# Performance work log

Measured on AMD Instinct MI355X. Metric: run time of the kernel, lower is better.

Reference implementation:

```python
import jax, jax.numpy as jnp
import numpy as np
from math import sqrt

B, S, D, H = 4, 2048, 1024, 16
DH = D // H          # 64
DF = 4 * D           # 4096
EPS = 1e-5
NEG = -1e9


def layer_norm(x, w, b):
    mu = jnp.mean(x, axis=-1, keepdims=True)
    var = jnp.mean((x - mu) ** 2, axis=-1, keepdims=True)
    return (x - mu) * jax.lax.rsqrt(var + EPS) * w + b


def setup_inputs() -> dict:
    key = jax.random.key(0)
    ks = jax.random.split(key, 16)
    s = 0.02
    return {
        "state": jax.random.normal(ks[0], (B, S, D), jnp.float32),
        "mask": jax.random.randint(ks[1], (B, S), 0, 2, jnp.int32),
        "ln1_w": jnp.ones((D,), jnp.float32),
        "ln1_b": jnp.zeros((D,), jnp.float32),
        "Wq": jax.random.normal(ks[2], (H, D, DH), jnp.float32) * s,
        "bq": jnp.zeros((H, DH), jnp.float32),
        "Wk": jax.random.normal(ks[3], (H, D, DH), jnp.float32) * s,
        "bk": jnp.zeros((H, DH), jnp.float32),
        "Wv": jax.random.normal(ks[4], (H, D, DH), jnp.float32) * s,
        "bv": jnp.zeros((H, DH), jnp.float32),
        "Wo": jax.random.normal(ks[5], (D, D), jnp.float32) * s,
        "bo": jnp.zeros((D,), jnp.float32),
        "ln2_w": jnp.ones((D,), jnp.float32),
        "ln2_b": jnp.zeros((D,), jnp.float32),
        "W1": jax.random.normal(ks[6], (D, DF), jnp.float32) * s,
        "b1": jnp.zeros((DF,), jnp.float32),
        "W2": jax.random.normal(ks[7], (DF, D), jnp.float32) * s,
        "b2": jnp.zeros((D,), jnp.float32),
    }


def reference(state, mask, ln1_w, ln1_b, Wq, bq, Wk, bk, Wv, bv, Wo, bo,
              ln2_w, ln2_b, W1, b1, W2, b2):
    # pre-norm attention block
    hidden = layer_norm(state, ln1_w, ln1_b)               # [B,S,D]
    q = jnp.einsum("bsd,hde->bhse", hidden, Wq) + bq[None, :, None, :]
    k = jnp.einsum("bsd,hde->bhse", hidden, Wk) + bk[None, :, None, :]
    v = jnp.einsum("bsd,hde->bhse", hidden, Wv) + bv[None, :, None, :]
    scores = jnp.einsum("bhse,bhte->bhst", q, k) / sqrt(DH)  # [B,H,S,S]
    scores = jnp.where(mask[:, None, None, :] == 0, NEG, scores)
    weights = jax.nn.softmax(scores, axis=-1)
    attended = jnp.einsum("bhst,bhte->bhse", weights, v)    # [B,H,S,DH]
    # concat heads in head order (matches torch cat over per-head outputs)
    attended = attended.transpose(0, 2, 1, 3).reshape(B, S, D)
    attn_out = attended @ Wo + bo
    output = state + attn_out
    # pre-norm FFN block (dropout=0 -> identity)
    hidden = layer_norm(output, ln2_w, ln2_b)
    ff = jax.nn.gelu(hidden @ W1 + b1, approximate=False) @ W2 + b2
    return output + ff
```

## Files before the change

### kernel.cpp

```cpp
#include <hip/hip_runtime.h>
#include <math.h>

#define B_  4
#define S_  2048
#define D_  1024
#define H_  16
#define DH_ 64
#define DF_ 4096
#define M_  8192

#define QSC 0.18033688011112042f

typedef __attribute__((ext_vector_type(8))) short bf8_t;
typedef __attribute__((ext_vector_type(4))) float f4_t;

#if defined(__has_builtin)
#if __has_builtin(__builtin_amdgcn_cvt_pk_bf16_f32)
#define HAVE_PKCVT 1
#endif
#if __has_builtin(__builtin_amdgcn_global_load_lds)
#define HAVE_ASYNC 1
#endif
#if __has_builtin(__builtin_amdgcn_exp2f)
#define EXP2F(x) __builtin_amdgcn_exp2f(x)
#else
#define EXP2F(x) __expf((x) * 0.69314718055994531f)
#endif
#else
#define EXP2F(x) __expf((x) * 0.69314718055994531f)
#endif

__device__ __forceinline__ unsigned pk_bf16(float lo, float hi) {
#ifdef HAVE_PKCVT
  auto r = __builtin_amdgcn_cvt_pk_bf16_f32(lo, hi);
  unsigned u; __builtin_memcpy(&u, &r, 4); return u;
#else
  union { float f; unsigned u; } a, b2; a.f = lo; b2.f = hi;
  unsigned ra = a.u + 0x7fffu + ((a.u >> 16) & 1u);
  unsigned rb = b2.u + 0x7fffu + ((b2.u >> 16) & 1u);
  return (ra >> 16) | (rb & 0xffff0000u);
#endif
}

__device__ __forceinline__ unsigned short f2bf(float x) {
  return (unsigned short)(pk_bf16(x, x) & 0xffffu);
}

__device__ __forceinline__ bf8_t upk8(unsigned u0, unsigned u1, unsigned u2, unsigned u3) {
  union { unsigned u[4]; bf8_t v; } c;
  c.u[0] = u0; c.u[1] = u1; c.u[2] = u2; c.u[3] = u3; return c.v;
}

__device__ __forceinline__ f4_t mfma32(bf8_t a, bf8_t b, f4_t c) {
  return __builtin_amdgcn_mfma_f32_16x16x32_bf16(a, b, c, 0, 0, 0);
}

__device__ __forceinline__ void async16(const void* g, void* l) {
#ifdef HAVE_ASYNC
  __builtin_amdgcn_global_load_lds((__attribute__((address_space(1))) void*)(g),
                                   (__attribute__((address_space(3))) void*)(l), 16, 0, 0);
#else
  *(uint4*)l = *(const uint4*)g;
#endif
}

__device__ __forceinline__ int sw(int row) { return row & 7; }


__global__ __launch_bounds__(256) void wtrans_kernel(const float* __restrict__ in,
                                                     unsigned short* __restrict__ out,
                                                     int K, int N) {
  const int k0 = blockIdx.x * 32, n0 = blockIdx.y * 32;
  __shared__ float t[32][33];
  const int tid = threadIdx.x;
#pragma unroll
  for (int i = 0; i < 4; i++) {
    int idx = i * 256 + tid; int r = idx >> 5, c = idx & 31;
    t[r][c] = in[(size_t)(k0 + r) * N + n0 + c];
  }
  __syncthreads();
#pragma unroll
  for (int i = 0; i < 4; i++) {
    int idx = i * 256 + tid; int r = idx >> 5, c = idx & 31;
    out[(size_t)(n0 + r) * K + k0 + c] = f2bf(t[c][r]);
  }
}

__global__ __launch_bounds__(256) void qkvpack_kernel(const float* __restrict__ Wq,
                                                      const float* __restrict__ Wk,
                                                      const float* __restrict__ Wv,
                                                      unsigned short* __restrict__ WqkvT) {
  const int z = blockIdx.z;
  const int sel = z >> 4, h = z & 15;
  const float* in = (sel == 0 ? Wq : sel == 1 ? Wk : Wv) + (size_t)h * D_ * DH_;
  const int k0 = blockIdx.x * 32, n0 = blockIdx.y * 32;
  __shared__ float t[32][33];
  const int tid = threadIdx.x;
#pragma unroll
  for (int i = 0; i < 4; i++) {
    int idx = i * 256 + tid; int r = idx >> 5, c = idx & 31;
    t[r][c] = in[(size_t)(k0 + r) * DH_ + n0 + c];
  }
  __syncthreads();
#pragma unroll
  for (int i = 0; i < 4; i++) {
    int idx = i * 256 + tid; int r = idx >> 5, c = idx & 31;
    int n = sel * 1024 + h * 64 + n0 + r;
    WqkvT[(size_t)n * D_ + k0 + c] = f2bf(t[c][r]);
  }
}

__global__ void biaspack_kernel(const float* __restrict__ bq, const float* __restrict__ bk,
                                const float* __restrict__ bv, float* __restrict__ bqkv) {
  int i = blockIdx.x * 256 + threadIdx.x;
  if (i < 3072) {
    int sel = i >> 10, j = i & 1023;
    const float* src = sel == 0 ? bq : sel == 1 ? bk : bv;
    bqkv[i] = src[j];
  }
}


__global__ __launch_bounds__(256) void ln_kernel(const float* __restrict__ x,
                                                 const float* __restrict__ w,
                                                 const float* __restrict__ bb,
                                                 unsigned short* __restrict__ out) {
  const int row = blockIdx.x;
  const float* xr = x + (size_t)row * D_;
  const int tid = threadIdx.x;
  float v[4]; float s = 0.f;
#pragma unroll
  for (int i = 0; i < 4; i++) { v[i] = xr[tid + i * 256]; s += v[i]; }
  __shared__ float red[8];
#pragma unroll
  for (int o = 32; o; o >>= 1) s += __shfl_xor(s, o, 64);
  const int wv = tid >> 6, ln = tid & 63;
  if (!ln) red[wv] = s;
  __syncthreads();
  float mean = (red[0] + red[1] + red[2] + red[3]) * (1.f / 1024.f);
  float s2 = 0.f;
#pragma unroll
  for (int i = 0; i < 4; i++) { float d = v[i] - mean; s2 += d * d; }
#pragma unroll
  for (int o = 32; o; o >>= 1) s2 += __shfl_xor(s2, o, 64);
  if (!ln) red[4 + wv] = s2;
  __syncthreads();
  float var = (red[4] + red[5] + red[6] + red[7]) * (1.f / 1024.f);
  float rstd = rsqrtf(var + 1e-5f);
#pragma unroll
  for (int i = 0; i < 4; i++) {
    int c = tid + i * 256;
    out[(size_t)row * D_ + c] = f2bf((v[i] - mean) * rstd * w[c] + bb[c]);
  }
}

__global__ __launch_bounds__(256) void ffn2red_kernel(float* __restrict__ out,
                                                      const float* __restrict__ P,
                                                      const float* __restrict__ resid,
                                                      const float* __restrict__ bias) {
  const size_t i = ((size_t)blockIdx.x * 256 + threadIdx.x) * 4;
  f4_t a  = *(const f4_t*)&out[i];
  f4_t p  = *(const f4_t*)&P[i];
  f4_t rr = *(const f4_t*)&resid[i];
  f4_t bb = *(const f4_t*)&bias[(int)(i & 1023)];
  *(f4_t*)&out[i] = a + p + rr + bb;
}

template <int EPI>
__global__ __launch_bounds__(256) void gemm_bt(const unsigned short* __restrict__ A,
                                               const unsigned short* __restrict__ Bt,
                                               const float* __restrict__ bias,
                                               const float* __restrict__ resid,
                                               unsigned short* __restrict__ outb,
                                               float* __restrict__ outf,
                                               int Ndim, int Kdim) {
  __shared__ __align__(16) unsigned short Asmem[4096];
  __shared__ __align__(16) unsigned short Bsmem[4096];
  const int tid = threadIdx.x;
  const int wave = tid >> 6, lane = tid & 63;
  const int quad = lane >> 4, l16 = lane & 15;
  const int wm = wave >> 1, wn = wave & 1;

  const int gx = gridDim.x;
  const int nwg = gx * (int)gridDim.y;
  const int lin = (int)blockIdx.y * gx + (int)blockIdx.x;
  const int swz = (lin & 7) * (nwg >> 3) + (lin >> 3);
  const int m0 = (swz / gx) * 128, n0 = (swz % gx) * 128;

  const f4_t fzero = {0.f, 0.f, 0.f, 0.f};
  f4_t acc[4][4];
#pragma unroll
  for (int i = 0; i < 4; i++)
#pragma unroll
    for (int j = 0; j < 4; j++) acc[i][j] = fzero;

  const int rowA = tid >> 2;
  const int kp = (tid & 3) * 8;

  for (int k0 = 0; k0 < Kdim; k0 += 32) {
    __syncthreads();
#pragma unroll
    for (int r = 0; r < 2; r++) {
      const int row = r * 64 + rowA;
      const int e = row * 32 + kp;
      async16(A  + (size_t)(m0 + row) * Kdim + k0 + kp, &Asmem[e]);
      async16(Bt + (size_t)(n0 + row) * Kdim + k0 + kp, &Bsmem[e]);
    }
    __syncthreads();

    bf8_t a[4], b[4];
#pragma unroll
    for (int i = 0; i < 4; i++) {
      a[i] = *(const bf8_t*)&Asmem[(wm * 64 + i * 16 + l16) * 32 + quad * 8];
      b[i] = *(const bf8_t*)&Bsmem[(wn * 64 + i * 16 + l16) * 32 + quad * 8];
    }
#pragma unroll
    for (int i = 0; i < 4; i++)
#pragma unroll
      for (int j = 0; j < 4; j++)
        acc[i][j] = mfma32(a[i], b[j], acc[i][j]);
  }

#pragma unroll
  for (int i = 0; i < 4; i++) {
#pragma unroll
    for (int j = 0; j < 4; j++) {
#pragma unroll
      for (int r = 0; r < 4; r++) {
        const int m = m0 + wm * 64 + i * 16 + quad * 4 + r;
        const int n = n0 + wn * 64 + j * 16 + l16;
        float v = acc[i][j][r] + bias[n];
        if constexpr (EPI == 2) v = 0.5f * v * (1.f + erff(v * 0.70710678118654752f));
        if constexpr (EPI == 1) {
          v += resid[(size_t)m * Ndim + n];
          outf[(size_t)m * Ndim + n] = v;
        } else {
          outb[(size_t)m * Ndim + n] = f2bf(v);
        }
      }
    }
  }
}

template <int EPI>
__global__ __launch_bounds__(512, 2) void gemm256(const unsigned short* __restrict__ A,
                                                  const unsigned short* __restrict__ Bt,
                                                  const float* __restrict__ bias,
                                                  const float* __restrict__ resid,
                                                  unsigned short* __restrict__ outb,
                                                  float* __restrict__ outf,
                                                  float* __restrict__ outf2,
                                                  unsigned short* __restrict__ vTout,
                                                  int Ndim, int Kdim, int Kstride) {
  __shared__ __align__(16) unsigned short Asm[32768];
  __shared__ __align__(16) unsigned short Bsm[32768];
  const int tid = threadIdx.x;
  const int wave = tid >> 6, lane = tid & 63;
  const int quad = lane >> 4, l16 = lane & 15;
  const int wm = wave >> 2, wn = wave & 3;

  const int gx = gridDim.x;
  const int nwg = gx * (int)gridDim.y;
  const int lin = (int)blockIdx.y * gx + (int)blockIdx.x;
  const int swz = (lin & 7) * (nwg >> 3) + (lin >> 3);
  const int m0 = (swz / gx) * 256, n0 = (swz % gx) * 256;
  const int kz = (int)blockIdx.z * Kdim;

  const int NT = Kdim >> 6;
  const int srow = lane >> 3, schk = lane & 7;

#define STAGE_A(t, row0) do {                                               \
    const int r_ = (row0) + srow;                                           \
    async16(A + (size_t)(m0 + r_) * Kstride + kz + (t) * 64 +               \
                ((schk ^ (r_ & 7)) << 3),                                   \
            &Asm[(((t) & 1) << 14) + ((row0) << 6)]); } while (0)
#define STAGE_B(t, row0) do {                                               \
    const int r_ = (row0) + srow;                                           \
    async16(Bt + (size_t)(n0 + r_) * Kstride + kz + (t) * 64 +              \
                 ((schk ^ (r_ & 7)) << 3),                                  \
            &Bsm[(((t) & 1) << 14) + ((row0) << 6)]); } while (0)
#define STAGE_FULL(t) do {                                                  \
    STAGE_A(t, wave * 8);       STAGE_A(t, 64 + wave * 8);                  \
    STAGE_A(t, 128 + wave * 8); STAGE_A(t, 192 + wave * 8);                 \
    STAGE_B(t, wave * 8);       STAGE_B(t, 64 + wave * 8);                  \
    STAGE_B(t, 128 + wave * 8); STAGE_B(t, 192 + wave * 8); } while (0)

#define AFR(bo, row, s) \
  (*(const bf8_t*)&Asm[(bo) + ((row) << 6) + ((((s) * 4 + quad) ^ ((row) & 7)) << 3)])
#define BFR(bo, row, s) \
  (*(const bf8_t*)&Bsm[(bo) + ((row) << 6) + ((((s) * 4 + quad) ^ ((row) & 7)) << 3)])

  const f4_t fzero = {0.f, 0.f, 0.f, 0.f};
  f4_t acc[8][4];
#pragma unroll
  for (int i = 0; i < 8; i++)
#pragma unroll
    for (int j = 0; j < 4; j++) acc[i][j] = fzero;

  STAGE_FULL(0);
  STAGE_FULL(1);
  asm volatile("s_waitcnt vmcnt(8)" ::: "memory");
  __builtin_amdgcn_s_barrier();

  const int ar0 = wm << 7;
  const int br0 = wn << 6;

  for (int t = 0; t < NT; ++t) {
    const int bo = (t & 1) << 14;
    const bool pf = (t + 2) < NT;
    const int t2 = t + 2;
    bf8_t a0[8], b0[4], a1[8], b1[4];

#pragma unroll
    for (int i = 0; i < 8; i++) a0[i] = AFR(bo, ar0 + i * 16 + l16, 0);
#pragma unroll
    for (int j = 0; j < 4; j++) b0[j] = BFR(bo, br0 + j * 16 + l16, 0);
#pragma unroll
    for (int i = 0; i < 8; i++) a1[i] = AFR(bo, ar0 + i * 16 + l16, 1);
#pragma unroll
    for (int j = 0; j < 4; j++) b1[j] = BFR(bo, br0 + j * 16 + l16, 1);

    __builtin_amdgcn_s_setprio(1);
#pragma unroll
    for (int i = 0; i < 8; i++)
#pragma unroll
      for (int j = 0; j < 4; j++)
        acc[i][j] = mfma32(a0[i], b0[j], acc[i][j]);
    __builtin_amdgcn_s_setprio(0);

    asm volatile("s_waitcnt lgkmcnt(0)" ::: "memory");
    __builtin_amdgcn_s_barrier();

    if (pf) STAGE_FULL(t2);

    __builtin_amdgcn_s_setprio(1);
#pragma unroll
    for (int i = 0; i < 8; i++)
#pragma unroll
      for (int j = 0; j < 4; j++)
        acc[i][j] = mfma32(a1[i], b1[j], acc[i][j]);
    __builtin_amdgcn_s_setprio(0);

    if (pf) asm volatile("s_waitcnt vmcnt(8)" ::: "memory");
    else    asm volatile("s_waitcnt vmcnt(0)" ::: "memory");
    __builtin_amdgcn_s_barrier();
  }

#undef STAGE_A
#undef STAGE_B
#undef STAGE_FULL
#undef AFR
#undef BFR

  if (EPI == 0 && n0 >= 2048) {
    const int bb2 = m0 >> 11;
    const int sb64 = (m0 & 2047) + (wm << 7);
#pragma unroll
    for (int mi = 0; mi < 8; mi++) {
      const int i4 = mi & 3;
      const int g0 = (i4 & 2) * 16 + 8 * quad + 4 * (i4 & 1);
      const int sbase = sb64 + (mi >> 2) * 64 + g0;
#pragma unroll
      for (int nj = 0; nj < 4; nj++) {
        const int n = n0 + wn * 64 + nj * 16 + l16;
        const int ef = n - 2048;
        const int hh = ef >> 6, e = ef & 63;
        const float bsv = bias[n];
        uint2 wq;
        wq.x = pk_bf16(acc[mi][nj][0] + bsv, acc[mi][nj][1] + bsv);
        wq.y = pk_bf16(acc[mi][nj][2] + bsv, acc[mi][nj][3] + bsv);
        *(uint2*)&vTout[(size_t)((bb2 * 16 + hh) * 64 + e) * S_ + sbase] = wq;
      }
    }
    return;
  }

  float* const pdst = (EPI == 3) ? (blockIdx.z ? outf2 : outf) : outf;
  const float sc = (EPI == 0 && n0 < 1024) ? QSC : 1.f;
#pragma unroll
  for (int mi = 0; mi < 8; mi++) {
#pragma unroll
    for (int nj = 0; nj < 4; nj++) {
      const int n = n0 + wn * 64 + nj * 16 + l16;
      const float bs = (EPI == 3) ? 0.f : bias[n];
#pragma unroll
      for (int r = 0; r < 4; r++) {
        const int m = m0 + wm * 128 + mi * 16 + quad * 4 + r;
        float v = acc[mi][nj][r] + bs;
        if constexpr (EPI == 0) v *= sc;
        if constexpr (EPI == 2) v = 0.5f * v * (1.f + erff(v * 0.70710678118654752f));
        if constexpr (EPI == 1) {
          v += resid[(size_t)m * Ndim + n];
          outf[(size_t)m * Ndim + n] = v;
        } else if constexpr (EPI == 3) {
          pdst[(size_t)m * Ndim + n] = v;
        } else {
          outb[(size_t)m * Ndim + n] = f2bf(v);
        }
      }
    }
  }
}


__global__ __launch_bounds__(256) void attn_kernel(const unsigned short* __restrict__ qkv,
                                                   const unsigned short* __restrict__ vT,
                                                   const int* __restrict__ maskp,
                                                   unsigned short* __restrict__ attended) {
  const int bh = blockIdx.y, b = bh >> 4, h = bh & 15;
  const int q0 = blockIdx.x * 128;
  const int tid = threadIdx.x, wv = tid >> 6, lane = tid & 63;
  const int quad = lane >> 4, l16 = lane & 15;
  __shared__ __align__(16) unsigned short smem[16384];
  __shared__ float biasl[128];
  unsigned short* Ks = smem;
  unsigned short* Vs = smem + 8192;

  bf8_t aq[2][2];
#pragma unroll
  for (int sb = 0; sb < 2; sb++) {
    const unsigned short* qrow =
        qkv + (size_t)(b * S_ + q0 + wv * 32 + sb * 16 + l16) * 3072 + h * 64;
    aq[sb][0] = *(const bf8_t*)(qrow + quad * 8);
    aq[sb][1] = *(const bf8_t*)(qrow + 32 + quad * 8);
  }

  const bf8_t ones8 = {0x3F80, 0x3F80, 0x3F80, 0x3F80, 0x3F80, 0x3F80, 0x3F80, 0x3F80};
  const f4_t fzero = {0.f, 0.f, 0.f, 0.f};
  f4_t o[2][4], lacc[2];
#pragma unroll
  for (int sb = 0; sb < 2; sb++) {
    lacc[sb] = fzero;
#pragma unroll
    for (int ee = 0; ee < 4; ee++) o[sb][ee] = fzero;
  }

  for (int t0 = 0; t0 < S_; t0 += 128) {
    __syncthreads();
#pragma unroll
    for (int r = 0; r < 4; r++) {
      int ci = r * 256 + tid;
      int krow = ci >> 3, kc = (ci & 7) ^ sw(krow);
      async16(qkv + (size_t)(b * S_ + t0 + krow) * 3072 + 1024 + h * 64 + kc * 8,
              &Ks[ci * 8]);
      int e = ci >> 4, half = (ci >> 3) & 1, vc = (ci & 7) ^ sw(e);
      async16(vT + (size_t)(bh * 64 + e) * S_ + t0 + half * 64 + vc * 8,
              &Vs[ci * 8]);
    }
    if (tid < 128) biasl[tid] = maskp[b * S_ + t0 + tid] ? 0.f : -8e9f;
    __syncthreads();

#pragma unroll
    for (int th = 0; th < 2; th++) {
      f4_t sf[2][4];
#pragma unroll
      for (int jj = 0; jj < 4; jj++) {
        f4_t bi = *(const f4_t*)&biasl[th * 64 + jj * 16 + quad * 4];
        sf[0][jj] = bi;
        sf[1][jj] = bi;
      }
#pragma unroll
      for (int jj = 0; jj < 4; jj++) {
        int krow = th * 64 + jj * 16 + l16, sk = sw(krow);
        bf8_t kf0 = *(const bf8_t*)&Ks[krow * 64 + (quad ^ sk) * 8];
        bf8_t kf1 = *(const bf8_t*)&Ks[krow * 64 + ((quad + 4) ^ sk) * 8];
        sf[0][jj] = mfma32(kf0, aq[0][0], sf[0][jj]);
        sf[0][jj] = mfma32(kf1, aq[0][1], sf[0][jj]);
        sf[1][jj] = mfma32(kf0, aq[1][0], sf[1][jj]);
        sf[1][jj] = mfma32(kf1, aq[1][1], sf[1][jj]);
      }

      bf8_t pp[2][2];
#pragma unroll
      for (int sb = 0; sb < 2; sb++) {
#pragma unroll
        for (int h2 = 0; h2 < 2; h2++) {
          float p0 = EXP2F(sf[sb][2 * h2][0]),     p1 = EXP2F(sf[sb][2 * h2][1]);
          float p2 = EXP2F(sf[sb][2 * h2][2]),     p3 = EXP2F(sf[sb][2 * h2][3]);
          float p4 = EXP2F(sf[sb][2 * h2 + 1][0]), p5 = EXP2F(sf[sb][2 * h2 + 1][1]);
          float p6 = EXP2F(sf[sb][2 * h2 + 1][2]), p7 = EXP2F(sf[sb][2 * h2 + 1][3]);
          pp[sb][h2] = upk8(pk_bf16(p0, p1), pk_bf16(p2, p3),
                            pk_bf16(p4, p5), pk_bf16(p6, p7));
        }
        lacc[sb] = mfma32(ones8, pp[sb][0], lacc[sb]);
        lacc[sb] = mfma32(ones8, pp[sb][1], lacc[sb]);
      }

#pragma unroll
      for (int ee = 0; ee < 4; ee++) {
        int vrow = ee * 16 + l16, sv = sw(vrow);
#pragma unroll
        for (int h2 = 0; h2 < 2; h2++) {
          bf8_t vf = *(const bf8_t*)&Vs[vrow * 128 + th * 64 + ((4 * h2 + quad) ^ sv) * 8];
          o[0][ee] = mfma32(vf, pp[0][h2], o[0][ee]);
          o[1][ee] = mfma32(vf, pp[1][h2], o[1][ee]);
        }
      }
    }
  }

  float linv[2];
#pragma unroll
  for (int sb = 0; sb < 2; sb++) linv[sb] = 1.f / lacc[sb][0];

  __syncthreads();
  unsigned short* Os = smem;
#pragma unroll
  for (int sb = 0; sb < 2; sb++) {
    int srow = wv * 32 + sb * 16 + l16;
#pragma unroll
    for (int ee = 0; ee < 4; ee++) {
      unsigned w0 = pk_bf16(o[sb][ee][0] * linv[sb], o[sb][ee][1] * linv[sb]);
      unsigned w1 = pk_bf16(o[sb][ee][2] * linv[sb], o[sb][ee][3] * linv[sb]);
      uint2 wq; wq.x = w0; wq.y = w1;
      *(uint2*)&Os[srow * 72 + ee * 16 + quad * 4] = wq;
    }
  }
  __syncthreads();
#pragma unroll
  for (int it = 0; it < 4; it++) {
    int row = it * 32 + (tid >> 3), e0 = (tid & 7) * 8;
    bf8_t v = *(const bf8_t*)&Os[row * 72 + e0];
    *(bf8_t*)&attended[(size_t)(b * S_ + q0 + row) * D_ + h * 64 + e0] = v;
  }
}


extern "C" void kernel_launch(void* const* d_in, const int* in_sizes, int n_in,
                              void* d_out, int out_size, void* d_ws, size_t ws_size,
                              hipStream_t stream) {
  const float* state = (const float*)d_in[0];
  const int*   maskp = (const int*)d_in[1];
  const float* ln1w  = (const float*)d_in[2];
  const float* ln1b  = (const float*)d_in[3];
  const float* Wq    = (const float*)d_in[4];
  const float* bq    = (const float*)d_in[5];
  const float* Wk    = (const float*)d_in[6];
  const float* bk    = (const float*)d_in[7];
  const float* Wv    = (const float*)d_in[8];
  const float* bv    = (const float*)d_in[9];
  const float* Wo    = (const float*)d_in[10];
  const float* bo    = (const float*)d_in[11];
  const float* ln2w  = (const float*)d_in[12];
  const float* ln2b  = (const float*)d_in[13];
  const float* W1    = (const float*)d_in[14];
  const float* b1    = (const float*)d_in[15];
  const float* W2    = (const float*)d_in[16];
  const float* b2    = (const float*)d_in[17];

  char* w = (char*)d_ws;
  unsigned short* hidden = (unsigned short*)w; w += (size_t)M_ * D_ * 2;
  unsigned short* WqkvT  = (unsigned short*)w; w += (size_t)3072 * D_ * 2;
  unsigned short* WoT    = (unsigned short*)w; w += (size_t)D_ * D_ * 2;
  unsigned short* W1T    = (unsigned short*)w; w += (size_t)DF_ * D_ * 2;
  unsigned short* qkv    = (unsigned short*)w; w += (size_t)M_ * 3072 * 2;
  unsigned short* vT     = (unsigned short*)w; w += (size_t)M_ * D_ * 2;
  float*          outp   = (float*)w;          w += (size_t)M_ * D_ * 4;
  unsigned short* W2T    = (unsigned short*)w; w += (size_t)D_ * DF_ * 2;
  float*          bqkv   = (float*)w;          w += 3072 * 4;
  unsigned short* ff1    = qkv;
  float*          Pbuf   = (float*)hidden;

  qkvpack_kernel<<<dim3(32, 2, 48), 256, 0, stream>>>(Wq, Wk, Wv, WqkvT);
  wtrans_kernel<<<dim3(32, 32), 256, 0, stream>>>(Wo, WoT, D_, D_);
  wtrans_kernel<<<dim3(32, 128), 256, 0, stream>>>(W1, W1T, D_, DF_);
  wtrans_kernel<<<dim3(128, 32), 256, 0, stream>>>(W2, W2T, DF_, D_);
  biaspack_kernel<<<12, 256, 0, stream>>>(bq, bk, bv, bqkv);

  ln_kernel<<<M_, 256, 0, stream>>>(state, ln1w, ln1b, hidden);
  gemm256<0><<<dim3(3072 / 256, M_ / 256), 512, 0, stream>>>(
      hidden, WqkvT, bqkv, nullptr, qkv, nullptr, nullptr, vT, 3072, D_, D_);
  attn_kernel<<<dim3(S_ / 128, B_ * H_), 256, 0, stream>>>(qkv, vT, maskp, hidden);
  gemm_bt<1><<<dim3(D_ / 128, M_ / 128), 256, 0, stream>>>(hidden, WoT, bo, state,
                                                           nullptr, outp, D_, D_);
  ln_kernel<<<M_, 256, 0, stream>>>(outp, ln2w, ln2b, hidden);
  gemm256<2><<<dim3(DF_ / 256, M_ / 256), 512, 0, stream>>>(
      hidden, W1T, b1, nullptr, ff1, nullptr, nullptr, nullptr, DF_, D_, D_);
  gemm256<3><<<dim3(D_ / 256, M_ / 256, 2), 512, 0, stream>>>(
      ff1, W2T, nullptr, nullptr, nullptr, Pbuf, (float*)d_out, nullptr,
      D_, DF_ / 2, DF_);
  ffn2red_kernel<<<(M_ * D_) / 1024, 256, 0, stream>>>((float*)d_out, Pbuf, outp, b2);
}
```

Measured before the change: 550.4 us.

## Double-buffer K/V tiles in attention with async prefetch and block swizzle

The attention kernel now double-buffers K and V tiles in LDS. The next tile's async global-to-LDS loads are issued before computing on the current one, with vmcnt-based waits in place of full syncs before each load. The mask bias for the whole sequence is precomputed once into LDS, blocks are remapped so co-scheduled blocks share a batch/head (better L2 reuse), and s_setprio boosts MFMA phases. LDS use roughly doubles, with launch_bounds(256,2) to keep occupancy, at the risk of subtle wait-count correctness.

```diff
diff --git a/kernel.cpp b/kernel.cpp
--- a/kernel.cpp
+++ b/kernel.cpp
@@ -403,18 +403,47 @@
 }
 
 
-__global__ __launch_bounds__(256) void attn_kernel(const unsigned short* __restrict__ qkv,
-                                                   const unsigned short* __restrict__ vT,
-                                                   const int* __restrict__ maskp,
-                                                   unsigned short* __restrict__ attended) {
-  const int bh = blockIdx.y, b = bh >> 4, h = bh & 15;
-  const int q0 = blockIdx.x * 128;
+__global__ __launch_bounds__(256, 2) void attn_kernel(const unsigned short* __restrict__ qkv,
+                                                      const unsigned short* __restrict__ vT,
+                                                      const int* __restrict__ maskp,
+                                                      unsigned short* __restrict__ attended) {
   const int tid = threadIdx.x, wv = tid >> 6, lane = tid & 63;
   const int quad = lane >> 4, l16 = lane & 15;
-  __shared__ __align__(16) unsigned short smem[16384];
-  __shared__ float biasl[128];
-  unsigned short* Ks = smem;
-  unsigned short* Vs = smem + 8192;
+
+  const int lin = (int)blockIdx.y * (int)gridDim.x + (int)blockIdx.x;
+  const int virt = (lin & 7) * 128 + (lin >> 3);
+  const int q0 = (virt & 15) * 128;
+  const int bh = virt >> 4, b = bh >> 4, h = bh & 15;
+
+  __shared__ __align__(16) unsigned short KsmF[16384];
+  __shared__ __align__(16) unsigned short VsmF[16384];
+  __shared__ float biasf[2048];
+
+  {
+    const int4 mk0 = *(const int4*)&maskp[b * S_ + tid * 8];
+    const int4 mk1 = *(const int4*)&maskp[b * S_ + tid * 8 + 4];
+    f4_t bv0, bv1;
+    bv0[0] = mk0.x ? 0.f : -8e9f; bv0[1] = mk0.y ? 0.f : -8e9f;
+    bv0[2] = mk0.z ? 0.f : -8e9f; bv0[3] = mk0.w ? 0.f : -8e9f;
+    bv1[0] = mk1.x ? 0.f : -8e9f; bv1[1] = mk1.y ? 0.f : -8e9f;
+    bv1[2] = mk1.z ? 0.f : -8e9f; bv1[3] = mk1.w ? 0.f : -8e9f;
+    *(f4_t*)&biasf[tid * 8] = bv0;
+    *(f4_t*)&biasf[tid * 8 + 4] = bv1;
+  }
+
+#define STAGE_T(it, cb) do {                                                   \
+    _Pragma("unroll")                                                          \
+    for (int r_ = 0; r_ < 4; r_++) {                                           \
+      const int cc = r_ * 256 + tid;                                           \
+      const int krow = cc >> 3, kc = (cc & 7) ^ (krow & 7);                    \
+      async16(qkv + (size_t)(b * S_ + (it) * 128 + krow) * 3072 + 1024 +       \
+                  h * 64 + kc * 8,                                             \
+              &KsmF[((cb) << 13) + cc * 8]);                                   \
+      const int e_ = cc >> 4, hf = (cc >> 3) & 1, vc = (cc & 7) ^ (e_ & 7);    \
+      async16(vT + (size_t)(bh * 64 + e_) * S_ + (it) * 128 + hf * 64 +        \
+                  vc * 8,                                                      \
+              &VsmF[((cb) << 13) + cc * 8]);                                   \
+    } } while (0)
 
   bf8_t aq[2][2];
 #pragma unroll
@@ -435,40 +464,42 @@
     for (int ee = 0; ee < 4; ee++) o[sb][ee] = fzero;
   }
 
-  for (int t0 = 0; t0 < S_; t0 += 128) {
-    __syncthreads();
-#pragma unroll
-    for (int r = 0; r < 4; r++) {
-      int ci = r * 256 + tid;
-      int krow = ci >> 3, kc = (ci & 7) ^ sw(krow);
-      async16(qkv + (size_t)(b * S_ + t0 + krow) * 3072 + 1024 + h * 64 + kc * 8,
-              &Ks[ci * 8]);
-      int e = ci >> 4, half = (ci >> 3) & 1, vc = (ci & 7) ^ sw(e);
-      async16(vT + (size_t)(bh * 64 + e) * S_ + t0 + half * 64 + vc * 8,
-              &Vs[ci * 8]);
-    }
-    if (tid < 128) biasl[tid] = maskp[b * S_ + t0 + tid] ? 0.f : -8e9f;
-    __syncthreads();
+  STAGE_T(0, 0);
+  asm volatile("s_waitcnt lgkmcnt(0)" ::: "memory");
+  __builtin_amdgcn_s_barrier();
+
+  for (int it = 0; it < S_ / 128; ++it) {
+    const int cb = it & 1;
+    __builtin_amdgcn_s_barrier();
+    if (it + 1 < S_ / 128) {
+      STAGE_T(it + 1, cb ^ 1);
+      asm volatile("s_waitcnt vmcnt(8)" ::: "memory");
+    } else {
+      asm volatile("s_waitcnt vmcnt(0)" ::: "memory");
+    }
+    __builtin_amdgcn_s_barrier();
 
 #pragma unroll
     for (int th = 0; th < 2; th++) {
       f4_t sf[2][4];
 #pragma unroll
       for (int jj = 0; jj < 4; jj++) {
-        f4_t bi = *(const f4_t*)&biasl[th * 64 + jj * 16 + quad * 4];
+        f4_t bi = *(const f4_t*)&biasf[it * 128 + th * 64 + jj * 16 + quad * 4];
         sf[0][jj] = bi;
         sf[1][jj] = bi;
       }
+      __builtin_amdgcn_s_setprio(1);
 #pragma unroll
       for (int jj = 0; jj < 4; jj++) {
-        int krow = th * 64 + jj * 16 + l16, sk = sw(krow);
-        bf8_t kf0 = *(const bf8_t*)&Ks[krow * 64 + (quad ^ sk) * 8];
-        bf8_t kf1 = *(const bf8_t*)&Ks[krow * 64 + ((quad + 4) ^ sk) * 8];
+        const int krow = th * 64 + jj * 16 + l16, sk = krow & 7;
+        bf8_t kf0 = *(const bf8_t*)&KsmF[(cb << 13) + krow * 64 + ((quad ^ sk) << 3)];
+        bf8_t kf1 = *(const bf8_t*)&KsmF[(cb << 13) + krow * 64 + (((quad + 4) ^ sk) << 3)];
         sf[0][jj] = mfma32(kf0, aq[0][0], sf[0][jj]);
         sf[0][jj] = mfma32(kf1, aq[0][1], sf[0][jj]);
         sf[1][jj] = mfma32(kf0, aq[1][0], sf[1][jj]);
         sf[1][jj] = mfma32(kf1, aq[1][1], sf[1][jj]);
       }
+      __builtin_amdgcn_s_setprio(0);
 
       bf8_t pp[2][2];
 #pragma unroll
@@ -486,25 +517,30 @@
         lacc[sb] = mfma32(ones8, pp[sb][1], lacc[sb]);
       }
 
+      __builtin_amdgcn_s_setprio(1);
 #pragma unroll
       for (int ee = 0; ee < 4; ee++) {
-        int vrow = ee * 16 + l16, sv = sw(vrow);
+        const int vrow = ee * 16 + l16, sv = vrow & 7;
 #pragma unroll
         for (int h2 = 0; h2 < 2; h2++) {
-          bf8_t vf = *(const bf8_t*)&Vs[vrow * 128 + th * 64 + ((4 * h2 + quad) ^ sv) * 8];
+          bf8_t vf = *(const bf8_t*)&VsmF[(cb << 13) + vrow * 128 +
+                                          (((4 * h2 + quad) ^ sv) << 3)
+                                          + th * 64];
           o[0][ee] = mfma32(vf, pp[0][h2], o[0][ee]);
           o[1][ee] = mfma32(vf, pp[1][h2], o[1][ee]);
         }
       }
-    }
-  }
+      __builtin_amdgcn_s_setprio(0);
+    }
+  }
+
+#undef STAGE_T
 
   float linv[2];
 #pragma unroll
   for (int sb = 0; sb < 2; sb++) linv[sb] = 1.f / lacc[sb][0];
 
   __syncthreads();
-  unsigned short* Os = smem;
 #pragma unroll
   for (int sb = 0; sb < 2; sb++) {
     int srow = wv * 32 + sb * 16 + l16;
@@ -513,14 +549,14 @@
       unsigned w0 = pk_bf16(o[sb][ee][0] * linv[sb], o[sb][ee][1] * linv[sb]);
       unsigned w1 = pk_bf16(o[sb][ee][2] * linv[sb], o[sb][ee][3] * linv[sb]);
       uint2 wq; wq.x = w0; wq.y = w1;
-      *(uint2*)&Os[srow * 72 + ee * 16 + quad * 4] = wq;
+      *(uint2*)&KsmF[srow * 72 + ee * 16 + quad * 4] = wq;
     }
   }
   __syncthreads();
 #pragma unroll
   for (int it = 0; it < 4; it++) {
     int row = it * 32 + (tid >> 3), e0 = (tid & 7) * 8;
-    bf8_t v = *(const bf8_t*)&Os[row * 72 + e0];
+    bf8_t v = *(const bf8_t*)&KsmF[row * 72 + e0];
     *(bf8_t*)&attended[(size_t)(b * S_ + q0 + row) * D_ + h * 64 + e0] = v;
   }
 }
```

Measured after the change: 644.2 us. 1.17x slower.
